# Kernel optimization log

Measured on AMD Instinct MI355X. Metric: run time of the kernel, lower is better.

Reference implementation:

```python
import jax, jax.numpy as jnp
import numpy as np


def setup_inputs() -> dict:
    key = jax.random.key(0)
    k1, k2, k3, k4 = jax.random.split(key, 4)
    B, T, D, H = 64, 256, 2048, 2048
    scale_w = 1.0 / np.sqrt(D)
    scale_h = 1.0 / np.sqrt(H)
    return {
        "x": jax.random.normal(k1, (B, T, D), dtype=jnp.float32),
        "W": jax.random.normal(k2, (D, H), dtype=jnp.float32) * scale_w,
        "Wh": jax.random.normal(k3, (H, H), dtype=jnp.float32) * scale_h,
        "b": jax.random.normal(k4, (H,), dtype=jnp.float32) * 0.01,
    }


def reference(x, W, Wh, b):
    """Elman RNN: h_t = tanh(x_t @ W + h_{t-1} @ Wh + b), h_0 = 0.
    return_sequences=False and activation=identity, so output is the final state.
    (The original computes step 0 with a zero state then loops t=1..T-1, which
    is exactly a scan over all T steps starting from h=0.)"""
    B, T, D = x.shape
    H = Wh.shape[0]
    # Precompute the input projection for all timesteps in one big GEMM.
    xw = jnp.einsum('btd,dh->tbh', x, W) + b  # [T, B, H]

    def step(h, xw_t):
        h = jnp.tanh(xw_t + h @ Wh)
        return h, None

    h0 = jnp.zeros((B, H), dtype=x.dtype)
    h_last, _ = jax.lax.scan(step, h0, xw)
    return h_last  # [B, H]
```

## Files before the change

### kernel.cpp

```cpp
#include <hip/hip_runtime.h>
#include <hip/hip_bf16.h>
#include <hip/hip_fp16.h>

typedef _Float16 f16;
typedef _Float16 f16x8 __attribute__((ext_vector_type(8)));
typedef float f32x4 __attribute__((ext_vector_type(4)));
typedef unsigned int u32;
typedef unsigned long long u64;

#define HB 2048
#define DD 2048
#define TT 256
#define BB 64

typedef const __attribute__((address_space(1))) u32 gu32;
typedef __attribute__((address_space(3))) u32 lu32;

__device__ __forceinline__ void gl_lds16(const void* g, void* l) {
    __builtin_amdgcn_global_load_lds((gu32*)g, (lu32*)l, 16, 0, 0);
}

#define LOADM_SC0(dst, ar)                                                    \
    asm volatile("global_load_dwordx4 %0, %8, off sc0\n\t"                    \
                 "global_load_dwordx4 %1, %8, off offset:64 sc0\n\t"          \
                 "global_load_dwordx4 %2, %8, off offset:128 sc0\n\t"         \
                 "global_load_dwordx4 %3, %8, off offset:192 sc0\n\t"         \
                 "global_load_dwordx4 %4, %8, off offset:256 sc0\n\t"         \
                 "global_load_dwordx4 %5, %8, off offset:320 sc0\n\t"         \
                 "global_load_dwordx4 %6, %8, off offset:384 sc0\n\t"         \
                 "global_load_dwordx4 %7, %8, off offset:448 sc0"             \
                 : "=&v"(dst[0]), "=&v"(dst[1]), "=&v"(dst[2]), "=&v"(dst[3]),\
                   "=&v"(dst[4]), "=&v"(dst[5]), "=&v"(dst[6]), "=&v"(dst[7]) \
                 : "v"(ar)                                                    \
                 : "memory")

#define VMCNT0 asm volatile("s_waitcnt vmcnt(0)" ::: "memory")
#define VMCNT4 asm volatile("s_waitcnt vmcnt(4)" ::: "memory")

__device__ __forceinline__ u32 ld_flag_sc0(const u32* p) {
    u32 v;
    asm volatile("global_load_dword %0, %1, off sc0\n\ts_waitcnt vmcnt(0)"
                 : "=v"(v) : "v"(p) : "memory");
    return v;
}
__device__ __forceinline__ u32 ld_flag_sc1(const u32* p) {
    u32 v;
    asm volatile("global_load_dword %0, %1, off sc1\n\ts_waitcnt vmcnt(0)"
                 : "=v"(v) : "v"(p) : "memory");
    return v;
}

__global__ __launch_bounds__(256) void k_transpose_cvt(const float* __restrict__ src,
                                                       f16* __restrict__ dst) {
    __shared__ f16 tile[64][65];
    int bx = blockIdx.x * 64;
    int by = blockIdx.y * 64;
    int tx = threadIdx.x & 63;
    int ty = threadIdx.x >> 6;
#pragma unroll
    for (int r = ty; r < 64; r += 4)
        tile[r][tx] = (f16)src[(size_t)(by + r) * HB + bx + tx];
    __syncthreads();
#pragma unroll
    for (int r = ty; r < 64; r += 4)
        dst[(size_t)(bx + r) * HB + by + tx] = tile[tx][r];
}

__global__ __launch_bounds__(256) void k_cvt_x(const float* __restrict__ x,
                                               f16* __restrict__ a16) {
    int r = blockIdx.x;
    int d = threadIdx.x * 8;
    const float* src = x + ((size_t)(r & 63) * TT + (r >> 6)) * DD + d;
    float4 v0 = *(const float4*)src;
    float4 v1 = *(const float4*)(src + 4);
    f16x8 o = {(f16)v0.x, (f16)v0.y, (f16)v0.z, (f16)v0.w,
               (f16)v1.x, (f16)v1.y, (f16)v1.z, (f16)v1.w};
    *(f16x8*)(a16 + (size_t)r * DD + d) = o;
}

__global__ __launch_bounds__(256) void k_gemm_xw_lds(const f16* __restrict__ a16,
                                                     const f16* __restrict__ W16T,
                                                     const float* __restrict__ bias,
                                                     f16* __restrict__ xw16) {
    __shared__ f16 As[128 * 32];
    __shared__ f16 Bs[128 * 32];
    int tid = threadIdx.x;
    int lane = tid & 63, w = tid >> 6;
    int wr = w >> 1, wc = w & 1;
    int lr = lane & 15, kg = lane >> 4;
    int rowBase = blockIdx.y * 128;
    int colBase = blockIdx.x * 128;

    f32x4 acc[4][4] = {};

    int r0 = tid >> 2, c0 = ((tid & 3) ^ ((r0 >> 1) & 3)) * 8;
    int u1 = tid + 256;
    int r1 = u1 >> 2, c1 = ((u1 & 3) ^ ((r1 >> 1) & 3)) * 8;
    const f16* gA0 = a16 + (size_t)(rowBase + r0) * DD + c0;
    const f16* gA1 = a16 + (size_t)(rowBase + r1) * DD + c1;
    const f16* gB0 = W16T + (size_t)(colBase + r0) * DD + c0;
    const f16* gB1 = W16T + (size_t)(colBase + r1) * DD + c1;
    f16* lA0 = As + (size_t)(w * 64) * 8;
    f16* lA1 = As + (size_t)(256 + w * 64) * 8;
    f16* lB0 = Bs + (size_t)(w * 64) * 8;
    f16* lB1 = Bs + (size_t)(256 + w * 64) * 8;

    for (int kk = 0; kk < DD; kk += 32) {
        gl_lds16(gA0 + kk, lA0);
        gl_lds16(gA1 + kk, lA1);
        gl_lds16(gB0 + kk, lB0);
        gl_lds16(gB1 + kk, lB1);
        __syncthreads();

        f16x8 af[4], bf[4];
#pragma unroll
        for (int mi = 0; mi < 4; ++mi) {
            int row = wr * 64 + mi * 16 + lr;
            af[mi] = *(const f16x8*)(As + row * 32 + (kg ^ ((row >> 1) & 3)) * 8);
        }
#pragma unroll
        for (int ni = 0; ni < 4; ++ni) {
            int rowb = wc * 64 + ni * 16 + lr;
            bf[ni] = *(const f16x8*)(Bs + rowb * 32 + (kg ^ ((rowb >> 1) & 3)) * 8);
        }
#pragma unroll
        for (int mi = 0; mi < 4; ++mi)
#pragma unroll
            for (int ni = 0; ni < 4; ++ni)
                acc[mi][ni] = __builtin_amdgcn_mfma_f32_16x16x32_f16(af[mi], bf[ni],
                                                                     acc[mi][ni], 0, 0, 0);
        __syncthreads();
    }

#pragma unroll
    for (int mi = 0; mi < 4; ++mi)
#pragma unroll
        for (int ni = 0; ni < 4; ++ni) {
            int col = colBase + wc * 64 + ni * 16 + lr;
            float bv = bias[col];
#pragma unroll
            for (int j = 0; j < 4; ++j) {
                int row = rowBase + wr * 64 + mi * 16 + kg * 4 + j;
                xw16[(size_t)row * HB + col] = (f16)(acc[mi][ni][j] + bv);
            }
        }
}

__global__ __launch_bounds__(256) void k_gemm_xw_direct(const float* __restrict__ x,
                                                        const f16* __restrict__ W16T,
                                                        const float* __restrict__ bias,
                                                        f16* __restrict__ xw16) {
    int lane = threadIdx.x & 63;
    int w = threadIdx.x >> 6;
    int wr = w >> 1, wc = w & 1;
    int rowBase = blockIdx.y * 64 + wr * 32;
    int colBase = blockIdx.x * 64 + wc * 32;
    int lr = lane & 15;
    int kg = lane >> 4;

    f32x4 acc[2][2] = {};

    int r0 = rowBase + lr;
    int r1 = rowBase + 16 + lr;
    const float* xrow0 = x + ((size_t)(r0 & 63) * TT + (r0 >> 6)) * DD;
    const float* xrow1 = x + ((size_t)(r1 & 63) * TT + (r1 >> 6)) * DD;
    const f16* wrow0 = W16T + (size_t)(colBase + lr) * DD;
    const f16* wrow1 = W16T + (size_t)(colBase + 16 + lr) * DD;

    for (int kk = 0; kk < DD; kk += 32) {
        int k = kk + kg * 8;
        const float4* pa0 = reinterpret_cast<const float4*>(xrow0 + k);
        const float4* pa1 = reinterpret_cast<const float4*>(xrow1 + k);
        float4 a0l = pa0[0], a0h = pa0[1];
        float4 a1l = pa1[0], a1h = pa1[1];
        f16x8 a0 = {(f16)a0l.x, (f16)a0l.y, (f16)a0l.z, (f16)a0l.w,
                    (f16)a0h.x, (f16)a0h.y, (f16)a0h.z, (f16)a0h.w};
        f16x8 a1 = {(f16)a1l.x, (f16)a1l.y, (f16)a1l.z, (f16)a1l.w,
                    (f16)a1h.x, (f16)a1h.y, (f16)a1h.z, (f16)a1h.w};
        f16x8 b0 = *reinterpret_cast<const f16x8*>(wrow0 + k);
        f16x8 b1 = *reinterpret_cast<const f16x8*>(wrow1 + k);
        acc[0][0] = __builtin_amdgcn_mfma_f32_16x16x32_f16(a0, b0, acc[0][0], 0, 0, 0);
        acc[0][1] = __builtin_amdgcn_mfma_f32_16x16x32_f16(a0, b1, acc[0][1], 0, 0, 0);
        acc[1][0] = __builtin_amdgcn_mfma_f32_16x16x32_f16(a1, b0, acc[1][0], 0, 0, 0);
        acc[1][1] = __builtin_amdgcn_mfma_f32_16x16x32_f16(a1, b1, acc[1][1], 0, 0, 0);
    }

#pragma unroll
    for (int mi = 0; mi < 2; ++mi)
#pragma unroll
        for (int ni = 0; ni < 2; ++ni) {
            int col = colBase + ni * 16 + lr;
            float bv = bias[col];
#pragma unroll
            for (int j = 0; j < 4; ++j) {
                int row = rowBase + mi * 16 + kg * 4 + j;
                xw16[(size_t)row * HB + col] = (f16)(acc[mi][ni][j] + bv);
            }
        }
}

__global__ __launch_bounds__(128) void k_rnn_step(const f16* __restrict__ hin,
                                                  const f16* __restrict__ WhT,
                                                  const f16* __restrict__ xw_t,
                                                  f16* __restrict__ hout,
                                                  float* __restrict__ dout, int last,
                                                  int first) {
    int lane = threadIdx.x & 63;
    int w = threadIdx.x >> 6;
    int m0 = blockIdx.y * 32 + w * 16;
    int n0 = blockIdx.x * 16;
    int lr = lane & 15;
    int kg = lane >> 4;

    f32x4 acc = {};
    if (!first) {
        const f16* arow = hin + (size_t)(m0 + lr) * HB;
        const f16* brow = WhT + (size_t)(n0 + lr) * HB;
#pragma unroll 4
        for (int kk = 0; kk < HB; kk += 32) {
            int k = kk + kg * 8;
            f16x8 a = *reinterpret_cast<const f16x8*>(arow + k);
            f16x8 b = *reinterpret_cast<const f16x8*>(brow + k);
            acc = __builtin_amdgcn_mfma_f32_16x16x32_f16(a, b, acc, 0, 0, 0);
        }
    }

#pragma unroll
    for (int j = 0; j < 4; ++j) {
        int row = m0 + kg * 4 + j;
        int col = n0 + lr;
        float pre = acc[j] + (float)xw_t[(size_t)row * HB + col];
        float h = tanhf(pre);
        hout[(size_t)row * HB + col] = (f16)h;
        if (last) dout[(size_t)row * HB + col] = h;
    }
}

__global__ __launch_bounds__(512, 2) void k_rnn_persist(const f16* __restrict__ Wh16T,
                                                        const f16* __restrict__ xw16,
                                                        f16* __restrict__ hseq,
                                                        float* __restrict__ dout,
                                                        u32* __restrict__ bar) {
    __shared__ float red[2][8][8][68];
    __shared__ u32 ready_s;
    __shared__ u32 role_s;
    volatile u32* ready = &ready_s;
    int tid = threadIdx.x;
    int lane = tid & 63, w = tid >> 6;
    int lr = lane & 15, kg = lane >> 4;

    u32* claim = bar + 16000;
    if (tid == 0) {
        *ready = 0;
        u32 xcd;
        asm volatile("s_getreg_b32 %0, hwreg(20, 0, 32)" : "=s"(xcd));
        xcd &= 7;
        u32 role = 0;
        for (int a = 0; a < 8; ++a) {
            u32 gg = (xcd + (u32)a) & 7;
            u32 n = __hip_atomic_fetch_add(&claim[gg], 1u, __ATOMIC_RELAXED,
                                           __HIP_MEMORY_SCOPE_AGENT);
            if (n < 32u) {
                role = (n << 3) | gg;
                break;
            }
        }
        role_s = role;
    }
    __syncthreads();
    u32 vbid = role_s;
    int g = (int)(vbid & 7);
    int j = (int)(vbid >> 3);
    int row0 = g * 8;
    int n0 = j * 64;

    f16x8 bfrag[4][8];
#pragma unroll
    for (int n = 0; n < 4; ++n) {
        const f16* brow = Wh16T + (size_t)(n0 + n * 16 + lr) * DD + w * 256 + kg * 8;
#pragma unroll
        for (int s = 0; s < 8; ++s) bfrag[n][s] = *(const f16x8*)(brow + s * 32);
    }

    int f_row = tid >> 4;
    int f_c = (tid & 15) * 4;

    const u32* myflag =
        bar + (size_t)(((((u32)(lane >> 1) << 3) | (u32)g) << 1) | (lane & 1)) * 16;
    u32* ourflag = bar + (size_t)((vbid << 1) | (u32)(w & 1)) * 16;

    __syncthreads();

    u64 xwv_next = 0;
    if (tid < 128)
        xwv_next = *(const u64*)(xw16 + ((size_t)0 * BB + row0 + f_row) * HB + n0 + f_c);

    for (int t = 0; t < TT; ++t) {
        u64 xwv = xwv_next;

        f32x4 acc[4] = {};
        if (t > 0) {
            if (w == 7) {
                u32 tgt = (u32)t;
                u32 v = ld_flag_sc0(myflag);
                int tries = 0;
                while (!__all(v >= tgt)) {
                    __builtin_amdgcn_s_sleep(1);
                    v = (++tries < 8) ? ld_flag_sc0(myflag) : ld_flag_sc1(myflag);
                }
                if (lane == 0) *ready = (u32)t;
            } else {
                while (*ready < (u32)t) {  }
            }
            __builtin_amdgcn_sched_barrier(0);

            if (tid < 128 && t + 1 < TT)
                xwv_next = *(const u64*)(xw16 +
                                         ((size_t)(t + 1) * BB + row0 + f_row) * HB +
                                         n0 + f_c);

            const f16* abase = hseq + ((size_t)(t - 1) * BB + row0 + (lr & 7)) * HB +
                               w * 256 + kg * 8;
            f16x8 hv[8];
            LOADM_SC0(hv, abase);
            VMCNT4;
            __builtin_amdgcn_sched_barrier(0);
            if (lr >= 8) {
#pragma unroll
                for (int s = 0; s < 4; ++s) hv[s] = (f16x8)(f16)0;
            }
#pragma unroll
            for (int s = 0; s < 4; ++s)
#pragma unroll
                for (int n = 0; n < 4; ++n)
                    acc[n] = __builtin_amdgcn_mfma_f32_16x16x32_f16(hv[s], bfrag[n][s],
                                                                    acc[n], 0, 0, 0);
            VMCNT0;
            __builtin_amdgcn_sched_barrier(0);
            if (lr >= 8) {
#pragma unroll
                for (int s = 4; s < 8; ++s) hv[s] = (f16x8)(f16)0;
            }
#pragma unroll
            for (int s = 4; s < 8; ++s)
#pragma unroll
                for (int n = 0; n < 4; ++n)
                    acc[n] = __builtin_amdgcn_mfma_f32_16x16x32_f16(hv[s], bfrag[n][s],
                                                                    acc[n], 0, 0, 0);
        } else {
            if (tid < 128)
                xwv_next = *(const u64*)(xw16 + ((size_t)1 * BB + row0 + f_row) * HB +
                                         n0 + f_c);
        }

        if (kg < 2) {
#pragma unroll
            for (int n = 0; n < 4; ++n)
#pragma unroll
                for (int jj = 0; jj < 4; ++jj)
                    red[t & 1][w][kg * 4 + jj][n * 16 + lr] = acc[n][jj];
        }
        __syncthreads();

        if (tid < 128) {
            float4 sum = {0.f, 0.f, 0.f, 0.f};
#pragma unroll
            for (int ww = 0; ww < 8; ++ww) {
                float4 v = *(const float4*)&red[t & 1][ww][f_row][f_c];
                sum.x += v.x; sum.y += v.y; sum.z += v.z; sum.w += v.w;
            }
            union { u64 q; f16 h[4]; } xwu;
            xwu.q = xwv;
            float h0 = tanhf(sum.x + (float)xwu.h[0]);
            float h1 = tanhf(sum.y + (float)xwu.h[1]);
            float h2 = tanhf(sum.z + (float)xwu.h[2]);
            float h3 = tanhf(sum.w + (float)xwu.h[3]);

            if (t == TT - 1) {
                float4 o = {h0, h1, h2, h3};
                *(float4*)(dout + (size_t)(row0 + f_row) * HB + n0 + f_c) = o;
            } else {
                union { u64 q; f16 h[4]; } ho;
                ho.h[0] = (f16)h0; ho.h[1] = (f16)h1;
                ho.h[2] = (f16)h2; ho.h[3] = (f16)h3;
                u64* dst = (u64*)(hseq + ((size_t)t * BB + row0 + f_row) * HB + n0 + f_c);
                *(volatile u64*)dst = ho.q;
                VMCNT0;
                if ((tid & 63) == 0)
                    *(volatile u32*)ourflag = (u32)(t + 1);
                __hip_atomic_store(dst, ho.q, __ATOMIC_RELAXED,
                                   __HIP_MEMORY_SCOPE_AGENT);
                VMCNT0;
                if ((tid & 63) == 0)
                    __hip_atomic_store(ourflag, (u32)(t + 1), __ATOMIC_RELAXED,
                                       __HIP_MEMORY_SCOPE_AGENT);
            }
        }
    }
}

extern "C" void kernel_launch(void* const* d_in, const int* in_sizes, int n_in,
                              void* d_out, int out_size, void* d_ws, size_t ws_size,
                              hipStream_t stream) {
    const float* x = (const float*)d_in[0];
    const float* W = (const float*)d_in[1];
    const float* Wh = (const float*)d_in[2];
    const float* bias = (const float*)d_in[3];
    float* dout = (float*)d_out;

    char* ws = (char*)d_ws;
    const size_t SZ_WT = (size_t)HB * DD * 2;
    const size_t SZ_H = (size_t)BB * HB * 2;
    const size_t SZ_XW = (size_t)TT * BB * HB * 2;
    const size_t OFF_W = 0;
    const size_t OFF_WH = OFF_W + SZ_WT;
    const size_t OFF_H01 = OFF_WH + SZ_WT;
    const size_t OFF_BAR = OFF_H01 + 2 * SZ_H;
    const size_t OFF_XW = OFF_BAR + 65536;
    const size_t OFF_HSEQ = OFF_XW + SZ_XW;
    const size_t NEED_FULL = OFF_HSEQ + SZ_XW;

    f16* W16T = (f16*)(ws + OFF_W);
    f16* Wh16T = (f16*)(ws + OFF_WH);
    f16* h0 = (f16*)(ws + OFF_H01);
    f16* h1 = (f16*)(ws + OFF_H01 + SZ_H);
    u32* bar = (u32*)(ws + OFF_BAR);
    f16* xw16 = (f16*)(ws + OFF_XW);
    f16* hseq = (f16*)(ws + OFF_HSEQ);

    dim3 tgrid(32, 32);
    k_transpose_cvt<<<tgrid, 256, 0, stream>>>(W, W16T);
    k_transpose_cvt<<<tgrid, 256, 0, stream>>>(Wh, Wh16T);

    if (ws_size >= NEED_FULL) {
        f16* x16 = hseq;
        k_cvt_x<<<TT * BB, 256, 0, stream>>>(x, x16);
        k_gemm_xw_lds<<<dim3(HB / 128, TT * BB / 128), 256, 0, stream>>>(x16, W16T, bias, xw16);
        hipMemsetAsync(bar, 0, 65536, stream);
        k_rnn_persist<<<256, 512, 0, stream>>>(Wh16T, xw16, hseq, dout, bar);
    } else {
        k_gemm_xw_direct<<<dim3(HB / 64, TT * BB / 64), 256, 0, stream>>>(x, W16T, bias, xw16);
        f16* hb[2] = {h0, h1};
        for (int t = 0; t < TT; ++t) {
            const f16* xwt = xw16 + (size_t)t * BB * HB;
            k_rnn_step<<<dim3(128, 2), 128, 0, stream>>>(hb[t & 1], Wh16T, xwt,
                                                         hb[(t + 1) & 1], dout,
                                                         t == TT - 1, t == 0);
        }
    }
}
```

Baseline: 1.466 ms.

## Use 4-slot hidden-state ring with separate fast and coherent shadow buffers and flags

The full T-step hidden-state sequence buffer is replaced by a 4-slot ring placed in the W16T workspace region, which is free once the input GEMM has run. The ring is kept as two copies: a plain copy read with sc0 loads and a shadow copy written with agent-scope atomics and read with sc1 loads. Each copy has its own flag array. Once a block's waiter escalates to the coherent path, it stays there and signals the other waves through a bit packed into the ready word. This is meant to shrink the working set so it stays cache-resident and to stop fast and safe reads from aliasing the same lines, at the cost of extra flag logic and relying on blocks never running more than a few steps apart.

Result: slower. 1.517 ms (+3.5%).

```diff
diff --git a/kernel.cpp b/kernel.cpp
--- a/kernel.cpp
+++ b/kernel.cpp
@@ -29,6 +29,20 @@
                  "global_load_dwordx4 %5, %8, off offset:320 sc0\n\t"         \
                  "global_load_dwordx4 %6, %8, off offset:384 sc0\n\t"         \
                  "global_load_dwordx4 %7, %8, off offset:448 sc0"             \
+                 : "=&v"(dst[0]), "=&v"(dst[1]), "=&v"(dst[2]), "=&v"(dst[3]),\
+                   "=&v"(dst[4]), "=&v"(dst[5]), "=&v"(dst[6]), "=&v"(dst[7]) \
+                 : "v"(ar)                                                    \
+                 : "memory")
+
+#define LOADM_SC1(dst, ar)                                                    \
+    asm volatile("global_load_dwordx4 %0, %8, off sc1\n\t"                    \
+                 "global_load_dwordx4 %1, %8, off offset:64 sc1\n\t"          \
+                 "global_load_dwordx4 %2, %8, off offset:128 sc1\n\t"         \
+                 "global_load_dwordx4 %3, %8, off offset:192 sc1\n\t"         \
+                 "global_load_dwordx4 %4, %8, off offset:256 sc1\n\t"         \
+                 "global_load_dwordx4 %5, %8, off offset:320 sc1\n\t"         \
+                 "global_load_dwordx4 %6, %8, off offset:384 sc1\n\t"         \
+                 "global_load_dwordx4 %7, %8, off offset:448 sc1"             \
                  : "=&v"(dst[0]), "=&v"(dst[1]), "=&v"(dst[2]), "=&v"(dst[3]),\
                    "=&v"(dst[4]), "=&v"(dst[5]), "=&v"(dst[6]), "=&v"(dst[7]) \
                  : "v"(ar)                                                    \
@@ -238,7 +252,8 @@
 
 __global__ __launch_bounds__(512, 2) void k_rnn_persist(const f16* __restrict__ Wh16T,
                                                         const f16* __restrict__ xw16,
-                                                        f16* __restrict__ hseq,
+                                                        f16* __restrict__ rplain,
+                                                        f16* __restrict__ rshadow,
                                                         float* __restrict__ dout,
                                                         u32* __restrict__ bar) {
     __shared__ float red[2][8][8][68];
@@ -249,7 +264,7 @@
     int lane = tid & 63, w = tid >> 6;
     int lr = lane & 15, kg = lane >> 4;
 
-    u32* claim = bar + 16000;
+    u32* claim = bar + 24576;
     if (tid == 0) {
         *ready = 0;
         u32 xcd;
@@ -285,44 +300,54 @@
     int f_row = tid >> 4;
     int f_c = (tid & 15) * 4;
 
-    const u32* myflag =
-        bar + (size_t)(((((u32)(lane >> 1) << 3) | (u32)g) << 1) | (lane & 1)) * 16;
-    u32* ourflag = bar + (size_t)((vbid << 1) | (u32)(w & 1)) * 16;
-
-    __syncthreads();
+    u32 myslot = ((((u32)(lane >> 1) << 3) | (u32)g) << 1) | (lane & 1);
+    const u32* myfast = bar + (size_t)myslot * 16;
+    const u32* mysafe = bar + 8192 + (size_t)myslot * 16;
+    u32 ourslot = (vbid << 1) | (u32)(w & 1);
+    u32* ourfast = bar + (size_t)ourslot * 16;
+    u32* oursafe = bar + 8192 + (size_t)ourslot * 16;
 
     u64 xwv_next = 0;
     if (tid < 128)
         xwv_next = *(const u64*)(xw16 + ((size_t)0 * BB + row0 + f_row) * HB + n0 + f_c);
 
+    u32 esc = 0;
+
     for (int t = 0; t < TT; ++t) {
         u64 xwv = xwv_next;
 
         f32x4 acc[4] = {};
+        int useshadow = 0;
         if (t > 0) {
             if (w == 7) {
                 u32 tgt = (u32)t;
-                u32 v = ld_flag_sc0(myflag);
+                u32 v = esc ? ld_flag_sc1(mysafe) : ld_flag_sc0(myfast);
                 int tries = 0;
                 while (!__all(v >= tgt)) {
                     __builtin_amdgcn_s_sleep(1);
-                    v = (++tries < 8) ? ld_flag_sc0(myflag) : ld_flag_sc1(myflag);
+                    if (!esc && ++tries >= 8) esc = 1;
+                    v = esc ? ld_flag_sc1(mysafe) : ld_flag_sc0(myfast);
                 }
-                if (lane == 0) *ready = (u32)t;
+                if (lane == 0) *ready = ((u32)t << 1) | esc;
             } else {
-                while (*ready < (u32)t) {  }
+                while ((*ready >> 1) < (u32)t) {  }
             }
             __builtin_amdgcn_sched_barrier(0);
+            useshadow = (w == 7) ? (int)esc : (int)(*ready & 1);
 
             if (tid < 128 && t + 1 < TT)
                 xwv_next = *(const u64*)(xw16 +
                                          ((size_t)(t + 1) * BB + row0 + f_row) * HB +
                                          n0 + f_c);
 
-            const f16* abase = hseq + ((size_t)(t - 1) * BB + row0 + (lr & 7)) * HB +
-                               w * 256 + kg * 8;
+            size_t roff = (size_t)((t - 1) & 3) * BB * HB +
+                          (size_t)(row0 + (lr & 7)) * HB + w * 256 + kg * 8;
             f16x8 hv[8];
-            LOADM_SC0(hv, abase);
+            if (useshadow) {
+                LOADM_SC1(hv, rshadow + roff);
+            } else {
+                LOADM_SC0(hv, rplain + roff);
+            }
             VMCNT4;
             __builtin_amdgcn_sched_barrier(0);
             if (lr >= 8) {
@@ -383,16 +408,17 @@
                 union { u64 q; f16 h[4]; } ho;
                 ho.h[0] = (f16)h0; ho.h[1] = (f16)h1;
                 ho.h[2] = (f16)h2; ho.h[3] = (f16)h3;
-                u64* dst = (u64*)(hseq + ((size_t)t * BB + row0 + f_row) * HB + n0 + f_c);
-                *(volatile u64*)dst = ho.q;
+                size_t woff = (size_t)(t & 3) * BB * HB +
+                              (size_t)(row0 + f_row) * HB + n0 + f_c;
+                *(volatile u64*)(rplain + woff) = ho.q;
                 VMCNT0;
                 if ((tid & 63) == 0)
-                    *(volatile u32*)ourflag = (u32)(t + 1);
-                __hip_atomic_store(dst, ho.q, __ATOMIC_RELAXED,
+                    *(volatile u32*)ourfast = (u32)(t + 1);
+                __hip_atomic_store((u64*)(rshadow + woff), ho.q, __ATOMIC_RELAXED,
                                    __HIP_MEMORY_SCOPE_AGENT);
                 VMCNT0;
                 if ((tid & 63) == 0)
-                    __hip_atomic_store(ourflag, (u32)(t + 1), __ATOMIC_RELAXED,
+                    __hip_atomic_store(oursafe, (u32)(t + 1), __ATOMIC_RELAXED,
                                        __HIP_MEMORY_SCOPE_AGENT);
             }
         }
@@ -412,13 +438,14 @@
     const size_t SZ_WT = (size_t)HB * DD * 2;
     const size_t SZ_H = (size_t)BB * HB * 2;
     const size_t SZ_XW = (size_t)TT * BB * HB * 2;
+    const size_t SZ_RING = (size_t)4 * BB * HB * 2;
     const size_t OFF_W = 0;
     const size_t OFF_WH = OFF_W + SZ_WT;
     const size_t OFF_H01 = OFF_WH + SZ_WT;
     const size_t OFF_BAR = OFF_H01 + 2 * SZ_H;
-    const size_t OFF_XW = OFF_BAR + 65536;
-    const size_t OFF_HSEQ = OFF_XW + SZ_XW;
-    const size_t NEED_FULL = OFF_HSEQ + SZ_XW;
+    const size_t OFF_XW = OFF_BAR + 131072;
+    const size_t OFF_X16 = OFF_XW + SZ_XW;
+    const size_t NEED_FULL = OFF_X16 + SZ_XW;
 
     f16* W16T = (f16*)(ws + OFF_W);
     f16* Wh16T = (f16*)(ws + OFF_WH);
@@ -426,18 +453,19 @@
     f16* h1 = (f16*)(ws + OFF_H01 + SZ_H);
     u32* bar = (u32*)(ws + OFF_BAR);
     f16* xw16 = (f16*)(ws + OFF_XW);
-    f16* hseq = (f16*)(ws + OFF_HSEQ);
+    f16* x16 = (f16*)(ws + OFF_X16);
+    f16* rplain = (f16*)(ws + OFF_W);
+    f16* rshadow = (f16*)(ws + OFF_W + SZ_RING);
 
     dim3 tgrid(32, 32);
     k_transpose_cvt<<<tgrid, 256, 0, stream>>>(W, W16T);
     k_transpose_cvt<<<tgrid, 256, 0, stream>>>(Wh, Wh16T);
 
     if (ws_size >= NEED_FULL) {
-        f16* x16 = hseq;
         k_cvt_x<<<TT * BB, 256, 0, stream>>>(x, x16);
         k_gemm_xw_lds<<<dim3(HB / 128, TT * BB / 128), 256, 0, stream>>>(x16, W16T, bias, xw16);
-        hipMemsetAsync(bar, 0, 65536, stream);
-        k_rnn_persist<<<256, 512, 0, stream>>>(Wh16T, xw16, hseq, dout, bar);
+        hipMemsetAsync(bar, 0, 131072, stream);
+        k_rnn_persist<<<256, 512, 0, stream>>>(Wh16T, xw16, rplain, rshadow, dout, bar);
     } else {
         k_gemm_xw_direct<<<dim3(HB / 64, TT * BB / 64), 256, 0, stream>>>(x, W16T, bias, xw16);
         f16* hb[2] = {h0, h1};
```
